# Kernel tuning notes

Hardware: AMD Instinct MI355X
Metric: run time of the kernel (lower is better)

## Reference

```python
import jax, jax.numpy as jnp
import numpy as np

B = 32768          # batch
SEQ, F = 128, 8    # input_seq_len_samples, num_features
D = SEQ * F        # flattened input dim = 1024
E = 16             # num_experts
H1 = 256           # expert hidden
H2 = H1 // 2       # 128
GH = 128           # gating hidden


def _init_linear(key, fan_in, shape_w, shape_b):
    # torch nn.Linear default: U(-1/sqrt(fan_in), 1/sqrt(fan_in))
    kw, kb = jax.random.split(key)
    lim = 1.0 / np.sqrt(fan_in)
    W = jax.random.uniform(kw, shape_w, jnp.float32, -lim, lim)
    b = jax.random.uniform(kb, shape_b, jnp.float32, -lim, lim)
    return W, b


def setup_inputs() -> dict:
    key = jax.random.key(0)
    ks = jax.random.split(key, 6)
    x = jax.random.normal(ks[0], (B, SEQ, F), jnp.float32)
    # stacked expert weights: [E, in, out] layout
    W1, b1 = _init_linear(ks[1], D, (E, D, H1), (E, H1))
    W2, b2 = _init_linear(ks[2], H1, (E, H1, H2), (E, H2))
    W3, b3 = _init_linear(ks[3], H2, (E, H2, 1), (E, 1))
    Wg1, bg1 = _init_linear(ks[4], D, (D, GH), (GH,))
    Wg2, bg2 = _init_linear(ks[5], GH, (GH, E), (E,))
    return {"x": x, "W1": W1, "b1": b1, "W2": W2, "b2": b2,
            "W3": W3, "b3": b3, "Wg1": Wg1, "bg1": bg1,
            "Wg2": Wg2, "bg2": bg2}


def reference(x, W1, b1, W2, b2, W3, b3, Wg1, bg1, Wg2, bg2):
    bsz = x.shape[0]
    flat_x = x.reshape(bsz, -1)                      # [B, D]
    # gating network
    g = jax.nn.relu(flat_x @ Wg1 + bg1)              # [B, GH]
    gating_logits = g @ Wg2 + bg2                    # [B, E]
    gating_weights = jax.nn.softmax(gating_logits, axis=1)
    # all experts as one batched GEMM stack
    h = jax.nn.relu(jnp.einsum('bd,edh->beh', flat_x, W1) + b1)   # [B,E,H1]
    h = jax.nn.relu(jnp.einsum('beh,ehk->bek', h, W2) + b2)       # [B,E,H2]
    expert_outputs = jnp.einsum('bek,eko->beo', h, W3) + b3       # [B,E,1]
    final_output = jnp.sum(gating_weights[:, :, None] * expert_outputs, axis=1)  # [B,1]
    return final_output, gating_weights
```

## Files before the change

kernel.cpp:

```cpp
#include <hip/hip_runtime.h>
#include <stdint.h>
#include <stddef.h>

typedef short bf16x8 __attribute__((ext_vector_type(8)));
typedef float f32x4 __attribute__((ext_vector_type(4)));

__device__ __forceinline__ unsigned short bf16rn(float f){
  unsigned int u = __builtin_bit_cast(unsigned int, f);
  u += 0x7fffu + ((u >> 16) & 1u);
  return (unsigned short)(u >> 16);
}

__device__ __forceinline__ void gll16(const void* gsrc, void* ldst){
  __builtin_amdgcn_global_load_lds((const __attribute__((address_space(1))) unsigned int*)gsrc,
                                   (__attribute__((address_space(3))) unsigned int*)ldst,
                                   16, 0, 0);
}

__device__ __forceinline__ void barfence(){
  asm volatile("" ::: "memory");
  __builtin_amdgcn_s_barrier();
  asm volatile("" ::: "memory");
}

__global__ __launch_bounds__(256) void k_cvt_w(const float* __restrict__ src,
                                               unsigned short* __restrict__ dst,
                                               int K, int N){
  __shared__ float t[32][33];
  int e = blockIdx.z, k0 = blockIdx.x * 32, n0 = blockIdx.y * 32;
  const float* s = src + (size_t)e * K * N;
  unsigned short* d = dst + (size_t)e * N * K;
  int tx = threadIdx.x, ty = threadIdx.y;
  #pragma unroll
  for (int j = 0; j < 4; j++)
    t[ty + j*8][tx] = s[(size_t)(k0 + ty + j*8) * N + n0 + tx];
  __syncthreads();
  #pragma unroll
  for (int j = 0; j < 4; j++){
    int n = ty + j*8;
    d[(size_t)(n0 + n) * K + k0 + tx] = bf16rn(t[tx][n]);
  }
}

__global__ __launch_bounds__(128) void k_gating(const float* __restrict__ x,
                                                unsigned short* __restrict__ xb,
                                                const unsigned short* __restrict__ wg1t,
                                                const float* __restrict__ bg1,
                                                const float* __restrict__ wg2,
                                                const float* __restrict__ bg2,
                                                float* __restrict__ gout, int chunk_base){
  __shared__ unsigned short As[32*64];
  __shared__ unsigned short Bs[128*64];
  __shared__ float gl[32][129];
  __shared__ float redg[32][17];
  const int t = threadIdx.x, wid = t >> 6, l = t & 63;
  const int m0 = blockIdx.x * 32;
  const int jb = l & 7, rsub = l >> 3;
  f32x4 acc[2][4];
  #pragma unroll
  for (int i=0;i<2;i++)
    #pragma unroll
    for (int j=0;j<4;j++) acc[i][j] = (f32x4)0.f;

  for (int kt = 0; kt < 16; kt++){
    int k0 = kt * 64;
    #pragma unroll
    for (int i = 0; i < 2; i++){
      int s = t + i*128;
      int row = s >> 3, sk = s & 7;
      const float4* px = (const float4*)(x + (size_t)(m0 + row)*1024 + k0 + sk*8);
      float4 u0 = px[0], u1 = px[1];
      union { unsigned short h[8]; uint4 u; bf16x8 v; } r;
      r.h[0]=bf16rn(u0.x); r.h[1]=bf16rn(u0.y); r.h[2]=bf16rn(u0.z); r.h[3]=bf16rn(u0.w);
      r.h[4]=bf16rn(u1.x); r.h[5]=bf16rn(u1.y); r.h[6]=bf16rn(u1.z); r.h[7]=bf16rn(u1.w);
      *(bf16x8*)(As + row*64 + ((sk ^ (row & 7)) << 3)) = r.v;
      *(uint4*)(xb + (size_t)(m0 + row)*1024 + k0 + sk*8) = r.u;
    }
    #pragma unroll
    for (int i = 0; i < 8; i++){
      int idx = wid*8 + i; int row = idx*8 + rsub;
      gll16(wg1t + (size_t)row*1024 + k0 + ((jb ^ (row & 7)) << 3), Bs + idx*512);
    }
    __syncthreads();
    #pragma unroll
    for (int ks = 0; ks < 2; ks++){
      int blk = ks*4 + (l >> 4);
      bf16x8 a[2], b[4];
      #pragma unroll
      for (int fi = 0; fi < 2; fi++){
        int r = fi*16 + (l & 15);
        a[fi] = *(const bf16x8*)(As + r*64 + ((blk ^ (r & 7)) << 3));
      }
      #pragma unroll
      for (int fj = 0; fj < 4; fj++){
        int r = wid*64 + fj*16 + (l & 15);
        b[fj] = *(const bf16x8*)(Bs + r*64 + ((blk ^ (r & 7)) << 3));
      }
      #pragma unroll
      for (int fi = 0; fi < 2; fi++)
        #pragma unroll
        for (int fj = 0; fj < 4; fj++)
          acc[fi][fj] = __builtin_amdgcn_mfma_f32_16x16x32_bf16(a[fi], b[fj], acc[fi][fj], 0, 0, 0);
    }
    __syncthreads();
  }
  #pragma unroll
  for (int fi = 0; fi < 2; fi++)
    #pragma unroll
    for (int fj = 0; fj < 4; fj++){
      int c = wid*64 + fj*16 + (l & 15);
      float bv = bg1[c];
      #pragma unroll
      for (int r = 0; r < 4; r++){
        int row = fi*16 + (l >> 4)*4 + r;
        float v = acc[fi][fj][r] + bv;
        gl[row][c] = v > 0.f ? v : 0.f;
      }
    }
  __syncthreads();

  {
    const int row = t & 31, kq = t >> 5;
    float p[16];
    #pragma unroll
    for (int e = 0; e < 16; e++) p[e] = 0.f;
    for (int k = kq*32; k < kq*32 + 32; k++){
      float g = gl[row][k];
      const float* w = wg2 + k*16;
      #pragma unroll
      for (int e = 0; e < 16; e++) p[e] += g * w[e];
    }
    #pragma unroll
    for (int e = 0; e < 16; e++) p[e] += __shfl_xor(p[e], 32);
    if (t >= 64 && t < 96){
      #pragma unroll
      for (int e = 0; e < 16; e++) redg[t - 64][e] = p[e];
    }
    __syncthreads();
    if (t < 32){
      float le[16];
      #pragma unroll
      for (int e = 0; e < 16; e++) le[e] = bg2[e] + p[e] + redg[t][e];
      float m = le[0];
      #pragma unroll
      for (int e = 1; e < 16; e++) m = fmaxf(m, le[e]);
      float s = 0.f;
      #pragma unroll
      for (int e = 0; e < 16; e++){ le[e] = __expf(le[e] - m); s += le[e]; }
      float inv = 1.f / s;
      float4* o = (float4*)(gout + (size_t)(chunk_base + m0 + t)*16);
      #pragma unroll
      for (int q = 0; q < 4; q++)
        o[q] = make_float4(le[4*q]*inv, le[4*q+1]*inv, le[4*q+2]*inv, le[4*q+3]*inv);
    }
  }
}

template<int I0, int J0>
__device__ __forceinline__ void mfma_quad(const bf16x8 (&A)[4][2], const bf16x8 (&Bv)[2][2],
                                          f32x4 (&acc)[8][4]){
  #pragma unroll
  for (int fi = 0; fi < 4; ++fi)
    #pragma unroll
    for (int ks = 0; ks < 2; ++ks){
      acc[I0+fi][J0]   = __builtin_amdgcn_mfma_f32_16x16x32_bf16(A[fi][ks], Bv[0][ks], acc[I0+fi][J0],   0,0,0);
      acc[I0+fi][J0+1] = __builtin_amdgcn_mfma_f32_16x16x32_bf16(A[fi][ks], Bv[1][ks], acc[I0+fi][J0+1], 0,0,0);
    }
}

__global__ __launch_bounds__(512, 2) void k_fused(const unsigned short* __restrict__ xb,
                                                  const unsigned short* __restrict__ w1t,
                                                  const float* __restrict__ b1,
                                                  const unsigned short* __restrict__ w2t,
                                                  const float* __restrict__ b2,
                                                  const float* __restrict__ w3,
                                                  const float* __restrict__ b3,
                                                  float* __restrict__ outE,
                                                  int chunkB){
  extern __shared__ __align__(16) char smem[];
  const int t = threadIdx.x;
  const int wid = t >> 6, l = t & 63;
  const int wrow = wid >> 2, wcol = wid & 3;
  const int l3 = l >> 3, l7 = l & 7, l15 = l & 15, l4 = l >> 4;

  const int bid = blockIdx.x;
  const int slot = bid >> 3;
  const int e = (bid & 7)*2 + (slot & 1);
  const int mt = slot >> 1;
  const int m0 = mt * 256, n0 = e * 256;

  auto STAGE = [&](int isB, int p, int h, int kt){
    const unsigned short* gb = isB ? (w1t + (size_t)(n0 + h*128) * 1024)
                                   : (xb  + (size_t)(m0 + h*128) * 1024);
    char* dbase = smem + ((p << 16) | (isB << 15) | (h << 14));
    #pragma unroll
    for (int j = 0; j < 2; j++){
      int r = j*64 + wid*8 + l3;
      size_t src = (size_t)r * 1024 + (size_t)kt*64 + (size_t)((l7 ^ (r & 7)) << 3);
      gll16(gb + src, dbase + j*8192 + wid*1024);
    }
  };
  auto LDA = [&](int p, int qm, int fi, int ks) -> bf16x8 {
    int row = qm*64 + fi*16 + l15;
    int kb = (((ks << 2) | l4) ^ (row & 7)) << 4;
    return *(const bf16x8*)(smem + (p << 16) + (wrow << 14) + row*128 + kb);
  };
  auto LDB = [&](int p, int qn, int fj, int ks) -> bf16x8 {
    int row = (wcol & 1)*64 + qn*32 + fj*16 + l15;
    int kb = (((ks << 2) | l4) ^ (row & 7)) << 4;
    return *(const bf16x8*)(smem + (p << 16) + 32768 + ((wcol >> 1) << 14) + row*128 + kb);
  };

  f32x4 acc[8][4];
  #pragma unroll
  for (int i = 0; i < 8; i++)
    #pragma unroll
    for (int j = 0; j < 4; j++) acc[i][j] = (f32x4)0.f;

  bf16x8 a0[4][2], a1[4][2], b0[2][2], b1v[2][2];

  STAGE(0,0,0,0); STAGE(1,0,0,0); STAGE(0,0,1,0); STAGE(1,0,1,0);
  STAGE(1,1,0,1); STAGE(0,1,0,1);
  asm volatile("s_waitcnt vmcnt(4)" ::: "memory");
  barfence();

  for (int it = 0; it < 8; ++it){
    const int t0 = 2*it, k1 = t0 + 1;
    int c2 = t0 + 2, c3 = t0 + 3;
    if (c2 > 15) c2 = 14;
    if (c3 > 15) c3 = 14;

    #pragma unroll
    for (int fi = 0; fi < 4; ++fi){ a0[fi][0] = LDA(0,0,fi,0); a0[fi][1] = LDA(0,0,fi,1); }
    #pragma unroll
    for (int fj = 0; fj < 2; ++fj){ b0[fj][0] = LDB(0,0,fj,0); b0[fj][1] = LDB(0,0,fj,1); }
    STAGE(1,1,1,k1);
    barfence();
    __builtin_amdgcn_s_setprio(1);
    mfma_quad<0,0>(a0, b0, acc);
    __builtin_amdgcn_s_setprio(0);
    barfence();

    #pragma unroll
    for (int fj = 0; fj < 2; ++fj){ b1v[fj][0] = LDB(0,1,fj,0); b1v[fj][1] = LDB(0,1,fj,1); }
    STAGE(0,1,1,k1);
    barfence();
    __builtin_amdgcn_s_setprio(1);
    mfma_quad<0,2>(a0, b1v, acc);
    __builtin_amdgcn_s_setprio(0);
    barfence();

    #pragma unroll
    for (int fi = 0; fi < 4; ++fi){ a1[fi][0] = LDA(0,1,fi,0); a1[fi][1] = LDA(0,1,fi,1); }
    STAGE(1,0,0,c2);
    barfence();
    __builtin_amdgcn_s_setprio(1);
    mfma_quad<4,2>(a1, b1v, acc);
    __builtin_amdgcn_s_setprio(0);
    barfence();

    STAGE(0,0,0,c2);
    barfence();
    __builtin_amdgcn_s_setprio(1);
    mfma_quad<4,0>(a1, b0, acc);
    __builtin_amdgcn_s_setprio(0);
    asm volatile("s_waitcnt vmcnt(4)" ::: "memory");
    barfence();

    #pragma unroll
    for (int fi = 0; fi < 4; ++fi){ a0[fi][0] = LDA(1,0,fi,0); a0[fi][1] = LDA(1,0,fi,1); }
    #pragma unroll
    for (int fj = 0; fj < 2; ++fj){ b0[fj][0] = LDB(1,0,fj,0); b0[fj][1] = LDB(1,0,fj,1); }
    STAGE(1,0,1,c2);
    barfence();
    __builtin_amdgcn_s_setprio(1);
    mfma_quad<0,0>(a0, b0, acc);
    __builtin_amdgcn_s_setprio(0);
    barfence();

    #pragma unroll
    for (int fj = 0; fj < 2; ++fj){ b1v[fj][0] = LDB(1,1,fj,0); b1v[fj][1] = LDB(1,1,fj,1); }
    STAGE(0,0,1,c2);
    barfence();
    __builtin_amdgcn_s_setprio(1);
    mfma_quad<0,2>(a0, b1v, acc);
    __builtin_amdgcn_s_setprio(0);
    barfence();

    #pragma unroll
    for (int fi = 0; fi < 4; ++fi){ a1[fi][0] = LDA(1,1,fi,0); a1[fi][1] = LDA(1,1,fi,1); }
    STAGE(1,1,0,c3);
    barfence();
    __builtin_amdgcn_s_setprio(1);
    mfma_quad<4,2>(a1, b1v, acc);
    __builtin_amdgcn_s_setprio(0);
    barfence();

    STAGE(0,1,0,c3);
    barfence();
    __builtin_amdgcn_s_setprio(1);
    mfma_quad<4,0>(a1, b0, acc);
    __builtin_amdgcn_s_setprio(0);
    asm volatile("s_waitcnt vmcnt(4)" ::: "memory");
    barfence();
  }

  __syncthreads();

  {
    float bv[4];
    #pragma unroll
    for (int fj = 0; fj < 4; ++fj) bv[fj] = b1[e*256 + wcol*64 + fj*16 + l15];
    #pragma unroll
    for (int fi = 0; fi < 8; ++fi)
      #pragma unroll
      for (int fj = 0; fj < 4; ++fj){
        const int col = wcol*64 + fj*16 + l15;
        #pragma unroll
        for (int r = 0; r < 4; ++r){
          const int row = wrow*128 + fi*16 + l4*4 + r;
          float v = acc[fi][fj][r] + bv[fj];
          v = v > 0.f ? v : 0.f;
          *(unsigned short*)(smem + row*512 + ((((col >> 3) ^ (row & 31))) << 4) + ((col & 7) << 1)) = bf16rn(v);
        }
      }
  }

  const unsigned short* w2e = w2t + (size_t)e*(128*256);
  auto STAGE_W2 = [&](int c, int q){
    char* dbase = smem + 131072 + q*16384;
    #pragma unroll
    for (int j = 0; j < 2; j++){
      int r = j*64 + wid*8 + l3;
      size_t src = (size_t)r*256 + (size_t)c*64 + (size_t)((l7 ^ (r & 7)) << 3);
      gll16(w2e + src, dbase + j*8192 + wid*1024);
    }
  };
  STAGE_W2(0, 0);
  __syncthreads();

  const int wr2 = wid >> 1, wc2 = wid & 1;
  f32x4 acc2[4][4];
  #pragma unroll
  for (int i = 0; i < 4; i++)
    #pragma unroll
    for (int j = 0; j < 4; j++) acc2[i][j] = (f32x4)0.f;

  float w3v[4], b2v[4];
  #pragma unroll
  for (int fj = 0; fj < 4; ++fj){
    int c = wc2*64 + fj*16 + l15;
    w3v[fj] = w3[e*128 + c];
    b2v[fj] = b2[e*128 + c];
  }

  for (int c = 0; c < 4; ++c){
    if (c < 3) STAGE_W2(c+1, (c+1)&1);
    bf16x8 a2[4][2], bb[4][2];
    #pragma unroll
    for (int fi = 0; fi < 4; ++fi)
      #pragma unroll
      for (int ks = 0; ks < 2; ++ks){
        int row = wr2*64 + fi*16 + l15;
        int sl = (c*8 + ks*4 + l4) ^ (row & 31);
        a2[fi][ks] = *(const bf16x8*)(smem + row*512 + (sl << 4));
      }
    #pragma unroll
    for (int fj = 0; fj < 4; ++fj)
      #pragma unroll
      for (int ks = 0; ks < 2; ++ks){
        int n = wc2*64 + fj*16 + l15;
        int sl = (ks*4 + l4) ^ (n & 7);
        bb[fj][ks] = *(const bf16x8*)(smem + 131072 + (c&1)*16384 + n*128 + (sl << 4));
      }
    __builtin_amdgcn_s_setprio(1);
    #pragma unroll
    for (int fi = 0; fi < 4; ++fi)
      #pragma unroll
      for (int fj = 0; fj < 4; ++fj)
        #pragma unroll
        for (int ks = 0; ks < 2; ++ks)
          acc2[fi][fj] = __builtin_amdgcn_mfma_f32_16x16x32_bf16(a2[fi][ks], bb[fj][ks], acc2[fi][fj], 0, 0, 0);
    __builtin_amdgcn_s_setprio(0);
    __syncthreads();
  }

  float* red = (float*)(smem + 131072);
  #pragma unroll
  for (int fi = 0; fi < 4; ++fi)
    #pragma unroll
    for (int r = 0; r < 4; ++r){
      float s = 0.f;
      #pragma unroll
      for (int fj = 0; fj < 4; ++fj){
        float v = acc2[fi][fj][r] + b2v[fj];
        v = v > 0.f ? v : 0.f;
        s += v * w3v[fj];
      }
      s += __shfl_xor(s, 1); s += __shfl_xor(s, 2);
      s += __shfl_xor(s, 4); s += __shfl_xor(s, 8);
      if (l15 == 0){
        int row = wr2*64 + fi*16 + l4*4 + r;
        red[row*2 + wc2] = s;
      }
    }
  __syncthreads();
  if (t < 256)
    outE[(size_t)e*chunkB + m0 + t] = red[t*2 + 0] + red[t*2 + 1] + b3[e];
}

__global__ __launch_bounds__(256) void k_stage2b(const float* __restrict__ outE,
                                                 float* __restrict__ dout,
                                                 int chunk_base, int chunkB, int Btot){
  int row = blockIdx.x*256 + threadIdx.x;
  int rowg = chunk_base + row;
  const float* g = dout + Btot + (size_t)rowg*16;
  float s = 0.f;
  #pragma unroll
  for (int e = 0; e < 16; e++) s += g[e] * outE[(size_t)e*chunkB + row];
  dout[rowg] = s;
}

extern "C" void kernel_launch(void* const* d_in, const int* in_sizes, int n_in,
                              void* d_out, int out_size, void* d_ws, size_t ws_size,
                              hipStream_t stream){
  const float* x   = (const float*)d_in[0];
  const float* W1  = (const float*)d_in[1];
  const float* b1  = (const float*)d_in[2];
  const float* W2  = (const float*)d_in[3];
  const float* b2  = (const float*)d_in[4];
  const float* W3  = (const float*)d_in[5];
  const float* b3  = (const float*)d_in[6];
  const float* Wg1 = (const float*)d_in[7];
  const float* bg1 = (const float*)d_in[8];
  const float* Wg2 = (const float*)d_in[9];
  const float* bg2 = (const float*)d_in[10];
  float* out = (float*)d_out;

  const int B = in_sizes[0] / 1024;

  char* ws = (char*)d_ws;
  size_t off = 0;
  auto alloc = [&](size_t bytes){ size_t p = off; off = (off + bytes + 255) & ~(size_t)255; return p; };
  size_t o_w1t  = alloc((size_t)16*256*1024*2);
  size_t o_w2t  = alloc((size_t)16*128*256*2);
  size_t o_wg1t = alloc((size_t)128*1024*2);
  size_t fixed = off;

  const int cands[6] = {1, 2, 4, 8, 16, 32};
  int nc = 32;
  for (int i = 0; i < 6; i++){
    size_t cB = (size_t)B / cands[i];
    if (fixed + cB*2112 + 4096 <= ws_size){ nc = cands[i]; break; }
  }
  int chunkB = B / nc;

  size_t o_xb = alloc((size_t)chunkB*1024*2);
  size_t o_oe = alloc((size_t)chunkB*16*4);

  unsigned short* w1t  = (unsigned short*)(ws + o_w1t);
  unsigned short* w2t  = (unsigned short*)(ws + o_w2t);
  unsigned short* wg1t = (unsigned short*)(ws + o_wg1t);
  unsigned short* xb   = (unsigned short*)(ws + o_xb);
  float*          oE   = (float*)(ws + o_oe);

  hipFuncSetAttribute(reinterpret_cast<const void*>(k_fused),
                      hipFuncAttributeMaxDynamicSharedMemorySize, 163840);

  k_cvt_w<<<dim3(32, 8, 16), dim3(32, 8), 0, stream>>>(W1, w1t, 1024, 256);
  k_cvt_w<<<dim3(8, 4, 16),  dim3(32, 8), 0, stream>>>(W2, w2t, 256, 128);
  k_cvt_w<<<dim3(32, 4, 1),  dim3(32, 8), 0, stream>>>(Wg1, wg1t, 1024, 128);

  for (int c = 0; c < nc; c++){
    int cb = c * chunkB;
    k_gating<<<chunkB/32, 128, 0, stream>>>(x + (size_t)cb*1024, xb, wg1t, bg1, Wg2, bg2, out + B, cb);
    k_fused<<<chunkB/16, 512, 163840, stream>>>(xb, w1t, b1, w2t, b2, W3, b3, oE, chunkB);
    k_stage2b<<<chunkB/256, 256, 0, stream>>>(oE, out, cb, chunkB, B);
  }
}
```

Baseline: 355.1 us.

## Make fused expert kernel persistent over multiple M tiles per block

The fused expert MLP kernel now launches a smaller grid in which each block loops over several 256-row batch tiles with a fixed stride, keeping the expert index fixed and hoisting the bias and W3 loads out of the loop. This cuts the number of blocks launched and the per-block setup cost, and keeps each block on one expert's weights across tiles, which may improve cache reuse. In exchange, fewer blocks give coarser load balancing and a larger tail effect if the grid does not divide evenly across the CUs.

```diff
diff --git a/kernel.cpp b/kernel.cpp
--- a/kernel.cpp
+++ b/kernel.cpp
@@ -176,28 +176,29 @@
                                                   const float* __restrict__ w3,
                                                   const float* __restrict__ b3,
                                                   float* __restrict__ outE,
-                                                  int chunkB){
+                                                  int chunkB, int iters, int mstride){
   extern __shared__ __align__(16) char smem[];
   const int t = threadIdx.x;
   const int wid = t >> 6, l = t & 63;
   const int wrow = wid >> 2, wcol = wid & 3;
   const int l3 = l >> 3, l7 = l & 7, l15 = l & 15, l4 = l >> 4;
 
-  const int bid = blockIdx.x;
-  const int slot = bid >> 3;
-  const int e = (bid & 7)*2 + (slot & 1);
-  const int mt = slot >> 1;
-  const int m0 = mt * 256, n0 = e * 256;
+  const int gb = blockIdx.x;
+  const int e = (gb & 7)*2 + ((gb >> 3) & 1);
+  const int mtb = gb >> 4;
+  const int n0 = e * 256;
+
+  int m0;
 
   auto STAGE = [&](int isB, int p, int h, int kt){
-    const unsigned short* gb = isB ? (w1t + (size_t)(n0 + h*128) * 1024)
-                                   : (xb  + (size_t)(m0 + h*128) * 1024);
+    const unsigned short* gb_ = isB ? (w1t + (size_t)(n0 + h*128) * 1024)
+                                    : (xb  + (size_t)(m0 + h*128) * 1024);
     char* dbase = smem + ((p << 16) | (isB << 15) | (h << 14));
     #pragma unroll
     for (int j = 0; j < 2; j++){
       int r = j*64 + wid*8 + l3;
       size_t src = (size_t)r * 1024 + (size_t)kt*64 + (size_t)((l7 ^ (r & 7)) << 3);
-      gll16(gb + src, dbase + j*8192 + wid*1024);
+      gll16(gb_ + src, dbase + j*8192 + wid*1024);
     }
   };
   auto LDA = [&](int p, int qm, int fi, int ks) -> bf16x8 {
@@ -211,202 +212,203 @@
     return *(const bf16x8*)(smem + (p << 16) + 32768 + ((wcol >> 1) << 14) + row*128 + kb);
   };
 
-  f32x4 acc[8][4];
-  #pragma unroll
-  for (int i = 0; i < 8; i++)
-    #pragma unroll
-    for (int j = 0; j < 4; j++) acc[i][j] = (f32x4)0.f;
-
-  bf16x8 a0[4][2], a1[4][2], b0[2][2], b1v[2][2];
-
-  STAGE(0,0,0,0); STAGE(1,0,0,0); STAGE(0,0,1,0); STAGE(1,0,1,0);
-  STAGE(1,1,0,1); STAGE(0,1,0,1);
-  asm volatile("s_waitcnt vmcnt(4)" ::: "memory");
-  barfence();
-
-  for (int it = 0; it < 8; ++it){
-    const int t0 = 2*it, k1 = t0 + 1;
-    int c2 = t0 + 2, c3 = t0 + 3;
-    if (c2 > 15) c2 = 14;
-    if (c3 > 15) c3 = 14;
-
-    #pragma unroll
-    for (int fi = 0; fi < 4; ++fi){ a0[fi][0] = LDA(0,0,fi,0); a0[fi][1] = LDA(0,0,fi,1); }
-    #pragma unroll
-    for (int fj = 0; fj < 2; ++fj){ b0[fj][0] = LDB(0,0,fj,0); b0[fj][1] = LDB(0,0,fj,1); }
-    STAGE(1,1,1,k1);
-    barfence();
-    __builtin_amdgcn_s_setprio(1);
-    mfma_quad<0,0>(a0, b0, acc);
-    __builtin_amdgcn_s_setprio(0);
-    barfence();
-
-    #pragma unroll
-    for (int fj = 0; fj < 2; ++fj){ b1v[fj][0] = LDB(0,1,fj,0); b1v[fj][1] = LDB(0,1,fj,1); }
-    STAGE(0,1,1,k1);
-    barfence();
-    __builtin_amdgcn_s_setprio(1);
-    mfma_quad<0,2>(a0, b1v, acc);
-    __builtin_amdgcn_s_setprio(0);
-    barfence();
-
-    #pragma unroll
-    for (int fi = 0; fi < 4; ++fi){ a1[fi][0] = LDA(0,1,fi,0); a1[fi][1] = LDA(0,1,fi,1); }
-    STAGE(1,0,0,c2);
-    barfence();
-    __builtin_amdgcn_s_setprio(1);
-    mfma_quad<4,2>(a1, b1v, acc);
-    __builtin_amdgcn_s_setprio(0);
-    barfence();
-
-    STAGE(0,0,0,c2);
-    barfence();
-    __builtin_amdgcn_s_setprio(1);
-    mfma_quad<4,0>(a1, b0, acc);
-    __builtin_amdgcn_s_setprio(0);
-    asm volatile("s_waitcnt vmcnt(4)" ::: "memory");
-    barfence();
-
-    #pragma unroll
-    for (int fi = 0; fi < 4; ++fi){ a0[fi][0] = LDA(1,0,fi,0); a0[fi][1] = LDA(1,0,fi,1); }
-    #pragma unroll
-    for (int fj = 0; fj < 2; ++fj){ b0[fj][0] = LDB(1,0,fj,0); b0[fj][1] = LDB(1,0,fj,1); }
-    STAGE(1,0,1,c2);
-    barfence();
-    __builtin_amdgcn_s_setprio(1);
-    mfma_quad<0,0>(a0, b0, acc);
-    __builtin_amdgcn_s_setprio(0);
-    barfence();
-
-    #pragma unroll
-    for (int fj = 0; fj < 2; ++fj){ b1v[fj][0] = LDB(1,1,fj,0); b1v[fj][1] = LDB(1,1,fj,1); }
-    STAGE(0,0,1,c2);
-    barfence();
-    __builtin_amdgcn_s_setprio(1);
-    mfma_quad<0,2>(a0, b1v, acc);
-    __builtin_amdgcn_s_setprio(0);
-    barfence();
-
-    #pragma unroll
-    for (int fi = 0; fi < 4; ++fi){ a1[fi][0] = LDA(1,1,fi,0); a1[fi][1] = LDA(1,1,fi,1); }
-    STAGE(1,1,0,c3);
-    barfence();
-    __builtin_amdgcn_s_setprio(1);
-    mfma_quad<4,2>(a1, b1v, acc);
-    __builtin_amdgcn_s_setprio(0);
-    barfence();
-
-    STAGE(0,1,0,c3);
-    barfence();
-    __builtin_amdgcn_s_setprio(1);
-    mfma_quad<4,0>(a1, b0, acc);
-    __builtin_amdgcn_s_setprio(0);
-    asm volatile("s_waitcnt vmcnt(4)" ::: "memory");
-    barfence();
-  }
-
-  __syncthreads();
-
-  {
-    float bv[4];
-    #pragma unroll
-    for (int fj = 0; fj < 4; ++fj) bv[fj] = b1[e*256 + wcol*64 + fj*16 + l15];
-    #pragma unroll
-    for (int fi = 0; fi < 8; ++fi)
-      #pragma unroll
-      for (int fj = 0; fj < 4; ++fj){
-        const int col = wcol*64 + fj*16 + l15;
-        #pragma unroll
-        for (int r = 0; r < 4; ++r){
-          const int row = wrow*128 + fi*16 + l4*4 + r;
-          float v = acc[fi][fj][r] + bv[fj];
-          v = v > 0.f ? v : 0.f;
-          *(unsigned short*)(smem + row*512 + ((((col >> 3) ^ (row & 31))) << 4) + ((col & 7) << 1)) = bf16rn(v);
-        }
-      }
-  }
-
   const unsigned short* w2e = w2t + (size_t)e*(128*256);
-  auto STAGE_W2 = [&](int c, int q){
-    char* dbase = smem + 131072 + q*16384;
-    #pragma unroll
-    for (int j = 0; j < 2; j++){
-      int r = j*64 + wid*8 + l3;
-      size_t src = (size_t)r*256 + (size_t)c*64 + (size_t)((l7 ^ (r & 7)) << 3);
-      gll16(w2e + src, dbase + j*8192 + wid*1024);
-    }
-  };
-  STAGE_W2(0, 0);
-  __syncthreads();
-
   const int wr2 = wid >> 1, wc2 = wid & 1;
-  f32x4 acc2[4][4];
-  #pragma unroll
-  for (int i = 0; i < 4; i++)
-    #pragma unroll
-    for (int j = 0; j < 4; j++) acc2[i][j] = (f32x4)0.f;
-
-  float w3v[4], b2v[4];
+  float w3v[4], b2v[4], bv1[4];
   #pragma unroll
   for (int fj = 0; fj < 4; ++fj){
     int c = wc2*64 + fj*16 + l15;
     w3v[fj] = w3[e*128 + c];
     b2v[fj] = b2[e*128 + c];
-  }
-
-  for (int c = 0; c < 4; ++c){
-    if (c < 3) STAGE_W2(c+1, (c+1)&1);
-    bf16x8 a2[4][2], bb[4][2];
+    bv1[fj] = b1[e*256 + wcol*64 + fj*16 + l15];
+  }
+  float* red = (float*)(smem + 131072);
+
+  for (int j = 0; j < iters; ++j){
+    const int mt = mtb + j * mstride;
+    m0 = mt * 256;
+
+    f32x4 acc[8][4];
+    #pragma unroll
+    for (int i = 0; i < 8; i++)
+      #pragma unroll
+      for (int jj = 0; jj < 4; jj++) acc[i][jj] = (f32x4)0.f;
+
+    bf16x8 a0[4][2], a1[4][2], b0[2][2], b1v[2][2];
+
+    STAGE(0,0,0,0); STAGE(1,0,0,0); STAGE(0,0,1,0); STAGE(1,0,1,0);
+    STAGE(1,1,0,1); STAGE(0,1,0,1);
+    asm volatile("s_waitcnt vmcnt(4)" ::: "memory");
+    barfence();
+
+    for (int it = 0; it < 8; ++it){
+      const int k1 = 2*it + 1;
+      int c2 = 2*it + 2, c3 = 2*it + 3;
+      if (c2 > 15) c2 = 14;
+      if (c3 > 15) c3 = 14;
+
+      #pragma unroll
+      for (int fi = 0; fi < 4; ++fi){ a0[fi][0] = LDA(0,0,fi,0); a0[fi][1] = LDA(0,0,fi,1); }
+      #pragma unroll
+      for (int fj = 0; fj < 2; ++fj){ b0[fj][0] = LDB(0,0,fj,0); b0[fj][1] = LDB(0,0,fj,1); }
+      STAGE(1,1,1,k1);
+      barfence();
+      __builtin_amdgcn_s_setprio(1);
+      mfma_quad<0,0>(a0, b0, acc);
+      __builtin_amdgcn_s_setprio(0);
+      barfence();
+
+      #pragma unroll
+      for (int fj = 0; fj < 2; ++fj){ b1v[fj][0] = LDB(0,1,fj,0); b1v[fj][1] = LDB(0,1,fj,1); }
+      STAGE(0,1,1,k1);
+      barfence();
+      __builtin_amdgcn_s_setprio(1);
+      mfma_quad<0,2>(a0, b1v, acc);
+      __builtin_amdgcn_s_setprio(0);
+      barfence();
+
+      #pragma unroll
+      for (int fi = 0; fi < 4; ++fi){ a1[fi][0] = LDA(0,1,fi,0); a1[fi][1] = LDA(0,1,fi,1); }
+      STAGE(1,0,0,c2);
+      barfence();
+      __builtin_amdgcn_s_setprio(1);
+      mfma_quad<4,2>(a1, b1v, acc);
+      __builtin_amdgcn_s_setprio(0);
+      barfence();
+
+      STAGE(0,0,0,c2);
+      barfence();
+      __builtin_amdgcn_s_setprio(1);
+      mfma_quad<4,0>(a1, b0, acc);
+      __builtin_amdgcn_s_setprio(0);
+      asm volatile("s_waitcnt vmcnt(4)" ::: "memory");
+      barfence();
+
+      #pragma unroll
+      for (int fi = 0; fi < 4; ++fi){ a0[fi][0] = LDA(1,0,fi,0); a0[fi][1] = LDA(1,0,fi,1); }
+      #pragma unroll
+      for (int fj = 0; fj < 2; ++fj){ b0[fj][0] = LDB(1,0,fj,0); b0[fj][1] = LDB(1,0,fj,1); }
+      STAGE(1,0,1,c2);
+      barfence();
+      __builtin_amdgcn_s_setprio(1);
+      mfma_quad<0,0>(a0, b0, acc);
+      __builtin_amdgcn_s_setprio(0);
+      barfence();
+
+      #pragma unroll
+      for (int fj = 0; fj < 2; ++fj){ b1v[fj][0] = LDB(1,1,fj,0); b1v[fj][1] = LDB(1,1,fj,1); }
+      STAGE(0,0,1,c2);
+      barfence();
+      __builtin_amdgcn_s_setprio(1);
+      mfma_quad<0,2>(a0, b1v, acc);
+      __builtin_amdgcn_s_setprio(0);
+      barfence();
+
+      #pragma unroll
+      for (int fi = 0; fi < 4; ++fi){ a1[fi][0] = LDA(1,1,fi,0); a1[fi][1] = LDA(1,1,fi,1); }
+      STAGE(1,1,0,c3);
+      barfence();
+      __builtin_amdgcn_s_setprio(1);
+      mfma_quad<4,2>(a1, b1v, acc);
+      __builtin_amdgcn_s_setprio(0);
+      barfence();
+
+      STAGE(0,1,0,c3);
+      barfence();
+      __builtin_amdgcn_s_setprio(1);
+      mfma_quad<4,0>(a1, b0, acc);
+      __builtin_amdgcn_s_setprio(0);
+      asm volatile("s_waitcnt vmcnt(4)" ::: "memory");
+      barfence();
+    }
+
+    __syncthreads();
+
+    #pragma unroll
+    for (int fi = 0; fi < 8; ++fi)
+      #pragma unroll
+      for (int fj = 0; fj < 4; ++fj){
+        const int col = wcol*64 + fj*16 + l15;
+        #pragma unroll
+        for (int r = 0; r < 4; ++r){
+          const int row = wrow*128 + fi*16 + l4*4 + r;
+          float v = acc[fi][fj][r] + bv1[fj];
+          v = v > 0.f ? v : 0.f;
+          *(unsigned short*)(smem + row*512 + ((((col >> 3) ^ (row & 31))) << 4) + ((col & 7) << 1)) = bf16rn(v);
+        }
+      }
+
+    auto STAGE_W2 = [&](int c, int q){
+      char* dbase = smem + 131072 + q*16384;
+      #pragma unroll
+      for (int jj = 0; jj < 2; jj++){
+        int r = jj*64 + wid*8 + l3;
+        size_t src = (size_t)r*256 + (size_t)c*64 + (size_t)((l7 ^ (r & 7)) << 3);
+        gll16(w2e + src, dbase + jj*8192 + wid*1024);
+      }
+    };
+    STAGE_W2(0, 0);
+    __syncthreads();
+
+    f32x4 acc2[4][4];
+    #pragma unroll
+    for (int i = 0; i < 4; i++)
+      #pragma unroll
+      for (int jj = 0; jj < 4; jj++) acc2[i][jj] = (f32x4)0.f;
+
+    for (int c = 0; c < 4; ++c){
+      if (c < 3) STAGE_W2(c+1, (c+1)&1);
+      bf16x8 a2[4][2], bb[4][2];
+      #pragma unroll
+      for (int fi = 0; fi < 4; ++fi)
+        #pragma unroll
+        for (int ks = 0; ks < 2; ++ks){
+          int row = wr2*64 + fi*16 + l15;
+          int sl = (c*8 + ks*4 + l4) ^ (row & 31);
+          a2[fi][ks] = *(const bf16x8*)(smem + row*512 + (sl << 4));
+        }
+      #pragma unroll
+      for (int fj = 0; fj < 4; ++fj)
+        #pragma unroll
+        for (int ks = 0; ks < 2; ++ks){
+          int n = wc2*64 + fj*16 + l15;
+          int sl = (ks*4 + l4) ^ (n & 7);
+          bb[fj][ks] = *(const bf16x8*)(smem + 131072 + (c&1)*16384 + n*128 + (sl << 4));
+        }
+      __builtin_amdgcn_s_setprio(1);
+      #pragma unroll
+      for (int fi = 0; fi < 4; ++fi)
+        #pragma unroll
+        for (int fj = 0; fj < 4; ++fj)
+          #pragma unroll
+          for (int ks = 0; ks < 2; ++ks)
+            acc2[fi][fj] = __builtin_amdgcn_mfma_f32_16x16x32_bf16(a2[fi][ks], bb[fj][ks], acc2[fi][fj], 0, 0, 0);
+      __builtin_amdgcn_s_setprio(0);
+      __syncthreads();
+    }
+
     #pragma unroll
     for (int fi = 0; fi < 4; ++fi)
       #pragma unroll
-      for (int ks = 0; ks < 2; ++ks){
-        int row = wr2*64 + fi*16 + l15;
-        int sl = (c*8 + ks*4 + l4) ^ (row & 31);
-        a2[fi][ks] = *(const bf16x8*)(smem + row*512 + (sl << 4));
-      }
-    #pragma unroll
-    for (int fj = 0; fj < 4; ++fj)
-      #pragma unroll
-      for (int ks = 0; ks < 2; ++ks){
-        int n = wc2*64 + fj*16 + l15;
-        int sl = (ks*4 + l4) ^ (n & 7);
-        bb[fj][ks] = *(const bf16x8*)(smem + 131072 + (c&1)*16384 + n*128 + (sl << 4));
-      }
-    __builtin_amdgcn_s_setprio(1);
-    #pragma unroll
-    for (int fi = 0; fi < 4; ++fi)
-      #pragma unroll
-      for (int fj = 0; fj < 4; ++fj)
-        #pragma unroll
-        for (int ks = 0; ks < 2; ++ks)
-          acc2[fi][fj] = __builtin_amdgcn_mfma_f32_16x16x32_bf16(a2[fi][ks], bb[fj][ks], acc2[fi][fj], 0, 0, 0);
-    __builtin_amdgcn_s_setprio(0);
-    __syncthreads();
-  }
-
-  float* red = (float*)(smem + 131072);
-  #pragma unroll
-  for (int fi = 0; fi < 4; ++fi)
-    #pragma unroll
-    for (int r = 0; r < 4; ++r){
-      float s = 0.f;
-      #pragma unroll
-      for (int fj = 0; fj < 4; ++fj){
-        float v = acc2[fi][fj][r] + b2v[fj];
-        v = v > 0.f ? v : 0.f;
-        s += v * w3v[fj];
-      }
-      s += __shfl_xor(s, 1); s += __shfl_xor(s, 2);
-      s += __shfl_xor(s, 4); s += __shfl_xor(s, 8);
-      if (l15 == 0){
-        int row = wr2*64 + fi*16 + l4*4 + r;
-        red[row*2 + wc2] = s;
-      }
-    }
-  __syncthreads();
-  if (t < 256)
-    outE[(size_t)e*chunkB + m0 + t] = red[t*2 + 0] + red[t*2 + 1] + b3[e];
+      for (int r = 0; r < 4; ++r){
+        float s = 0.f;
+        #pragma unroll
+        for (int fj = 0; fj < 4; ++fj){
+          float v = acc2[fi][fj][r] + b2v[fj];
+          v = v > 0.f ? v : 0.f;
+          s += v * w3v[fj];
+        }
+        s += __shfl_xor(s, 1); s += __shfl_xor(s, 2);
+        s += __shfl_xor(s, 4); s += __shfl_xor(s, 8);
+        if (l15 == 0){
+          int row = wr2*64 + fi*16 + l4*4 + r;
+          red[row*2 + wc2] = s;
+        }
+      }
+    __syncthreads();
+    if (t < 256)
+      outE[(size_t)e*chunkB + m0 + t] = red[t*2 + 0] + red[t*2 + 1] + b3[e];
+  }
 }
 
 __global__ __launch_bounds__(256) void k_stage2b(const float* __restrict__ outE,
@@ -471,10 +473,15 @@
   k_cvt_w<<<dim3(8, 4, 16),  dim3(32, 8), 0, stream>>>(W2, w2t, 256, 128);
   k_cvt_w<<<dim3(32, 4, 1),  dim3(32, 8), 0, stream>>>(Wg1, wg1t, 1024, 128);
 
+  const int tiles = chunkB / 256;
+  const int iters = (tiles % 8 == 0) ? 8 : 1;
+  const int mstride = tiles / iters;
+  const int grid_f = 16 * mstride;
+
   for (int c = 0; c < nc; c++){
     int cb = c * chunkB;
     k_gating<<<chunkB/32, 128, 0, stream>>>(x + (size_t)cb*1024, xb, wg1t, bg1, Wg2, bg2, out + B, cb);
-    k_fused<<<chunkB/16, 512, 163840, stream>>>(xb, w1t, b1, w2t, b2, W3, b3, oE, chunkB);
+    k_fused<<<grid_f, 512, 163840, stream>>>(xb, w1t, b1, w2t, b2, W3, b3, oE, chunkB, iters, mstride);
     k_stage2b<<<chunkB/256, 256, 0, stream>>>(oE, out, cb, chunkB, B);
   }
 }
```

Measured after the change: 628.6 us. 1.77x slower.
